# Performance work log

Hardware: AMD Instinct MI355X
Metric: run time of the kernel (lower is better)

Reference implementation:

```python
import jax, jax.numpy as jnp
import numpy as np

TOP_K = 2
EPS = 1e-6

def setup_inputs() -> dict:
    key = jax.random.key(0)
    ks = jax.random.split(key, 4)
    B, L, D, E, ED = 2, 2048, 2048, 8, 2048
    scale_gu = (6.0 / D) ** 0.5   # kaiming_uniform-ish bound
    scale_dn = (6.0 / ED) ** 0.5
    return {
        "x": jax.random.normal(ks[0], (B, L, D), jnp.float32),
        "router_scale": jnp.ones((D,), jnp.float32),
        "gate_w": jax.random.normal(ks[1], (D, E), jnp.float32) * (D ** -0.5),
        "gate_up": jax.random.uniform(ks[2], (E, D, 2 * ED), jnp.float32, -scale_gu, scale_gu),
        "down": jax.random.uniform(ks[3], (E, ED, D), jnp.float32, -scale_dn, scale_dn),
        "per_expert_scale": jnp.ones((E,), jnp.float32),
    }

def reference(x, router_scale, gate_w, gate_up, down, per_expert_scale):
    B, L, D = x.shape
    E = gate_up.shape[0]
    # --- Router: RMSNorm (no scale) * D^-0.5 * router_scale -> linear -> softmax -> topk -> renorm
    h = x * jax.lax.rsqrt(jnp.mean(x * x, axis=-1, keepdims=True) + EPS)
    h = h * (D ** -0.5) * router_scale
    logits = (h @ gate_w).astype(jnp.float32)            # [B,L,E]
    probs = jax.nn.softmax(logits, axis=-1)
    w, idx = jax.lax.top_k(probs, TOP_K)                 # [B,L,K]
    w = w / jnp.clip(jnp.sum(w, axis=-1, keepdims=True), 1e-12)
    w = w.astype(x.dtype)
    # --- Experts: dense compute over all experts, weighted combine by routing
    N = B * L
    xf = x.reshape(N, D)
    idxf = idx.reshape(N, TOP_K)
    wf = w.reshape(N, TOP_K)
    # combine[n,e] = sum_k wf[n,k] * (idxf[n,k]==e); top_k indices are distinct per token
    combine = jnp.zeros((N, E), x.dtype).at[jnp.arange(N)[:, None], idxf].add(wf)
    hh = jnp.einsum('nd,edf->nef', xf, gate_up)          # [N,E,2*ED]
    gate, up = jnp.split(hh, 2, axis=-1)
    act = jax.nn.gelu(gate, approximate=False) * up      # [N,E,ED]
    y = jnp.einsum('nef,efd->ned', act, down)            # [N,E,D]
    out = jnp.einsum('ne,ned->nd', combine * per_expert_scale, y)
    return out.reshape(B, L, D)
```

## Files before the change

### kernel.cpp

```cpp
#include <hip/hip_runtime.h>
#include <hip/hip_bf16.h>
#include <math.h>

#define NTOK 4096
#define DM   2048
#define NE   8
#define BK2  32
#define NT   64
#define TILE_BYTES 32768
#define B_OFF      16384

using f32x4  = float __attribute__((ext_vector_type(4)));
using bf16x8 = __bf16 __attribute__((ext_vector_type(8)));
using u32x4  = unsigned int __attribute__((ext_vector_type(4)));

#define SBAR()  __builtin_amdgcn_s_barrier()
#define SCHED() __builtin_amdgcn_sched_barrier(0)

__device__ __forceinline__ unsigned short bf16bits(float f){
  unsigned u = __builtin_bit_cast(unsigned, f);
  return (unsigned short)((u + 0x7fffu + ((u >> 16) & 1u)) >> 16);
}

__device__ __forceinline__ void load_lds16(const void* g, void* l){
  __builtin_amdgcn_global_load_lds(
      (const __attribute__((address_space(1))) unsigned int*)g,
      (__attribute__((address_space(3))) unsigned int*)l, 16, 0, 0);
}

__global__ __launch_bounds__(256) void router_kernel(
    const float* __restrict__ x, const float* __restrict__ rs,
    const float* __restrict__ gw, const float* __restrict__ pes,
    unsigned short* __restrict__ xbf, int* __restrict__ cnt,
    int* __restrict__ toklist, float* __restrict__ slotw,
    int* __restrict__ tok2slot)
{
  const int wv = threadIdx.x >> 6, l = threadIdx.x & 63;
  const int n = blockIdx.x * 4 + wv;
  const float* xr = x + (size_t)n * DM;
  unsigned short* xb = xbf + (size_t)n * DM;
  float ssq = 0.f;
  float lg[8] = {0,0,0,0,0,0,0,0};
  #pragma unroll
  for (int q = 0; q < 8; ++q){
    int c4 = l + 64 * q;
    float4 v = ((const float4*)xr)[c4];
    float4 r = ((const float4*)rs)[c4];
    ssq += v.x*v.x + v.y*v.y + v.z*v.z + v.w*v.w;
    ushort4 o; o.x = bf16bits(v.x); o.y = bf16bits(v.y); o.z = bf16bits(v.z); o.w = bf16bits(v.w);
    ((ushort4*)xb)[c4] = o;
    float xs0 = v.x*r.x, xs1 = v.y*r.y, xs2 = v.z*r.z, xs3 = v.w*r.w;
    const float4* gp = (const float4*)(gw + (size_t)c4 * 32);
    float4 ga, gb;
    ga = gp[0]; gb = gp[1];
    lg[0]+=xs0*ga.x; lg[1]+=xs0*ga.y; lg[2]+=xs0*ga.z; lg[3]+=xs0*ga.w;
    lg[4]+=xs0*gb.x; lg[5]+=xs0*gb.y; lg[6]+=xs0*gb.z; lg[7]+=xs0*gb.w;
    ga = gp[2]; gb = gp[3];
    lg[0]+=xs1*ga.x; lg[1]+=xs1*ga.y; lg[2]+=xs1*ga.z; lg[3]+=xs1*ga.w;
    lg[4]+=xs1*gb.x; lg[5]+=xs1*gb.y; lg[6]+=xs1*gb.z; lg[7]+=xs1*gb.w;
    ga = gp[4]; gb = gp[5];
    lg[0]+=xs2*ga.x; lg[1]+=xs2*ga.y; lg[2]+=xs2*ga.z; lg[3]+=xs2*ga.w;
    lg[4]+=xs2*gb.x; lg[5]+=xs2*gb.y; lg[6]+=xs2*gb.z; lg[7]+=xs2*gb.w;
    ga = gp[6]; gb = gp[7];
    lg[0]+=xs3*ga.x; lg[1]+=xs3*ga.y; lg[2]+=xs3*ga.z; lg[3]+=xs3*ga.w;
    lg[4]+=xs3*gb.x; lg[5]+=xs3*gb.y; lg[6]+=xs3*gb.z; lg[7]+=xs3*gb.w;
  }
  #pragma unroll
  for (int off = 32; off; off >>= 1){
    ssq += __shfl_xor(ssq, off, 64);
    #pragma unroll
    for (int e2 = 0; e2 < 8; ++e2) lg[e2] += __shfl_xor(lg[e2], off, 64);
  }
  if (l == 0){
    float c = rsqrtf(ssq * (1.0f/DM) + 1e-6f) * 0.022097086912079608f;
    float mx = -1e30f;
    #pragma unroll
    for (int e2 = 0; e2 < 8; ++e2){ lg[e2] *= c; mx = fmaxf(mx, lg[e2]); }
    float l0 = lg[0]; int i0 = 0;
    #pragma unroll
    for (int e2 = 1; e2 < 8; ++e2) if (lg[e2] > l0){ l0 = lg[e2]; i0 = e2; }
    int i1 = (i0 == 0) ? 1 : 0; float l1 = (i0 == 0) ? lg[1] : lg[0];
    #pragma unroll
    for (int e2 = 0; e2 < 8; ++e2){ if (e2 != i0 && lg[e2] > l1){ l1 = lg[e2]; i1 = e2; } }
    float p0 = expf(l0 - mx), p1 = expf(l1 - mx);
    float sw = fmaxf(p0 + p1, 1e-12f);
    float w0 = p0 / sw, w1 = p1 / sw;
    int s0 = atomicAdd(&cnt[i0], 1);
    toklist[i0 * NTOK + s0] = n;
    slotw[i0 * NTOK + s0] = w0 * pes[i0];
    tok2slot[2 * n] = (i0 << 16) | s0;
    int s1 = atomicAdd(&cnt[i1], 1);
    toklist[i1 * NTOK + s1] = n;
    slotw[i1 * NTOK + s1] = w1 * pes[i1];
    tok2slot[2 * n + 1] = (i1 << 16) | s1;
  }
}

__global__ void scan_kernel(const int* __restrict__ cnt, int* __restrict__ basep){
  if (threadIdx.x == 0){
    int a = 0;
    for (int e = 0; e < NE; ++e){ basep[e] = a; a += cnt[e]; }
  }
}

__global__ __launch_bounds__(256) void conv_transpose_kernel(
    const float* __restrict__ W, unsigned short* __restrict__ Wt, int ncols)
{
  const int z = blockIdx.z;
  const float* src = W + (size_t)z * 2048 * ncols;
  unsigned short* dst = Wt + (size_t)z * ncols * 2048;
  const int n0 = blockIdx.x * 64, k0 = blockIdx.y * 64;
  __shared__ __align__(16) unsigned short t[64][72];
  const int tid = threadIdx.x;
  const int kl = tid >> 4;
  const int nl = (tid & 15) * 4;
  #pragma unroll
  for (int q = 0; q < 4; ++q){
    int k = kl + q * 16;
    float4 v = *(const float4*)(src + (size_t)(k0 + k) * ncols + n0 + nl);
    t[nl+0][k] = bf16bits(v.x);
    t[nl+1][k] = bf16bits(v.y);
    t[nl+2][k] = bf16bits(v.z);
    t[nl+3][k] = bf16bits(v.w);
  }
  __syncthreads();
  const int nr = tid >> 3;
  const int k8 = (tid & 7) * 8;
  #pragma unroll
  for (int q = 0; q < 2; ++q){
    int n = nr + q * 32;
    u32x4 v = *(const u32x4*)&t[n][k8];
    *(u32x4*)(dst + (size_t)(n0 + n) * 2048 + k0 + k8) = v;
  }
}

template<int MODE>
__global__ __launch_bounds__(512, 1) void moe_gemm(
    const unsigned short* __restrict__ Abuf,
    const unsigned short* __restrict__ Wt,
    unsigned short* __restrict__ act,
    unsigned short* __restrict__ ybuf,
    const int* __restrict__ cnt,
    const int* __restrict__ basep,
    const int* __restrict__ toklist,
    int e0)
{
  const int gx = gridDim.x, gy = gridDim.y, gz = gridDim.z;
  int flat = blockIdx.x + gx * (blockIdx.y + gy * blockIdx.z);
  int per  = (gx * gy * gz) >> 3;
  int id2  = (flat & 7) * per + (flat >> 3);
  int fpb  = gy * gz;
  int fbi  = id2 / fpb;
  int rem  = id2 % fpb;
  const int z  = rem / gy;
  const int e  = e0 + z;
  const int ce = cnt[e];
  const int m0 = (rem % gy) * 256;
  if (m0 >= ce) return;
  const int fb = fbi * (MODE == 0 ? 128 : 256);
  const int tid = threadIdx.x;
  const int l = tid & 63;
  const int wv = tid >> 6;
  const int wr = wv >> 2;
  const int wc = wv & 3;
  const int baseE = basep[e];
  const size_t ncols = (MODE == 0) ? 4096 : 2048;
  const unsigned short* Wz = Wt + (size_t)z * ncols * 2048;

  __shared__ __align__(16) unsigned short smem[4 * TILE_BYTES / 2];

  const unsigned short* asrc[2];
  #pragma unroll
  for (int q = 0; q < 2; ++q){
    int r = q * 128 + (tid >> 2);
    int g = (tid & 3) ^ ((r >> 1) & 3);
    long rsrc;
    if (MODE == 0) rsrc = toklist[e * NTOK + min(m0 + r, ce - 1)];
    else           rsrc = baseE + min(m0 + r, ce - 1);
    asrc[q] = Abuf + (size_t)rsrc * 2048 + g * 8;
  }
  const unsigned short* bsrc[2];
  #pragma unroll
  for (int q = 0; q < 2; ++q){
    int col = q * 128 + (tid >> 2);
    int g = (tid & 3) ^ ((col >> 1) & 3);
    int n;
    if (MODE == 0){ int sub = col & 63; n = fb + (col >> 6) * 32 + (sub & 31) + ((sub & 32) ? 2048 : 0); }
    else n = fb + col;
    bsrc[q] = Wz + (size_t)n * 2048 + g * 8;
  }
  const int ldst = tid * 16;

  const int kq = l >> 4;
  const int swz = (kq ^ (((l & 15) >> 1) & 3)) * 16;
  const int abase = (wr * 128 + (l & 15)) * 64 + swz;
  const int bbase = B_OFF + (wc * 64 + (l & 15)) * 64 + swz;

  f32x4 acc[8][4];
  #pragma unroll
  for (int i = 0; i < 8; ++i)
    #pragma unroll
    for (int j = 0; j < 4; ++j)
      acc[i][j] = (f32x4){0.f, 0.f, 0.f, 0.f};

  auto stage_a = [&](int buf, int st){
    char* base = (char*)smem + buf * TILE_BYTES;
    load_lds16(asrc[0] + st * BK2, base + ldst);
    load_lds16(asrc[1] + st * BK2, base + 8192 + ldst);
  };
  auto stage_b = [&](int buf, int st){
    char* base = (char*)smem + buf * TILE_BYTES + B_OFF;
    load_lds16(bsrc[0] + st * BK2, base + ldst);
    load_lds16(bsrc[1] + st * BK2, base + 8192 + ldst);
  };

  stage_a(0, 0); stage_b(0, 0);
  stage_a(1, 1); stage_b(1, 1);
  stage_a(2, 2); stage_b(2, 2);
  asm volatile("s_waitcnt vmcnt(8)");
  SCHED();
  SBAR();
  SCHED();

  #pragma unroll 1
  for (int kt = 0; kt < NT; ++kt){
    const char* C = (const char*)smem + (kt & 3) * TILE_BYTES;
    const int sb = (kt + 3) & 3;
    const int st = min(kt + 3, NT - 1);
    bf16x8 af[4], bfr[4];
    #pragma unroll
    for (int ni = 0; ni < 4; ++ni) bfr[ni] = *(const bf16x8*)(C + bbase + ni * 1024);
    #pragma unroll
    for (int mi = 0; mi < 4; ++mi) af[mi] = *(const bf16x8*)(C + abase + mi * 1024);
    stage_a(sb, st);
    SCHED();
    SBAR();
    SCHED();
    __builtin_amdgcn_s_setprio(1);
    #pragma unroll
    for (int ni = 0; ni < 4; ++ni)
      #pragma unroll
      for (int mi = 0; mi < 4; ++mi)
        acc[mi][ni] = __builtin_amdgcn_mfma_f32_16x16x32_bf16(af[mi], bfr[ni], acc[mi][ni], 0, 0, 0);
    __builtin_amdgcn_s_setprio(0);
    SCHED();
    SBAR();
    SCHED();
    #pragma unroll
    for (int mi = 0; mi < 4; ++mi) af[mi] = *(const bf16x8*)(C + abase + (mi + 4) * 1024);
    stage_b(sb, st);
    SCHED();
    SBAR();
    SCHED();
    __builtin_amdgcn_s_setprio(1);
    #pragma unroll
    for (int ni = 0; ni < 4; ++ni)
      #pragma unroll
      for (int mi = 0; mi < 4; ++mi)
        acc[mi + 4][ni] = __builtin_amdgcn_mfma_f32_16x16x32_bf16(af[mi], bfr[ni], acc[mi + 4][ni], 0, 0, 0);
    __builtin_amdgcn_s_setprio(0);
    SCHED();
    asm volatile("s_waitcnt vmcnt(8)");
    SCHED();
    SBAR();
    SCHED();
  }
  asm volatile("s_waitcnt vmcnt(0)");
  SCHED();

  const int lq4 = (l >> 4) * 4;
  if (MODE == 0){
    #pragma unroll
    for (int mi = 0; mi < 8; ++mi)
      #pragma unroll
      for (int j = 0; j < 4; ++j){
        int s = m0 + wr * 128 + mi * 16 + lq4 + j;
        if (s < ce){
          size_t rowb = (size_t)(baseE + s) * 2048;
          #pragma unroll
          for (int p = 0; p < 2; ++p){
            float g = acc[mi][p][j];
            float u = acc[mi][p + 2][j];
            float a = 0.5f * g * (1.0f + erff(g * 0.70710678118654752f)) * u;
            act[rowb + fb + wc * 32 + p * 16 + (l & 15)] = bf16bits(a);
          }
        }
      }
  } else {
    #pragma unroll
    for (int mi = 0; mi < 8; ++mi)
      #pragma unroll
      for (int j = 0; j < 4; ++j){
        int s = m0 + wr * 128 + mi * 16 + lq4 + j;
        if (s < ce){
          unsigned short* yr = ybuf + (size_t)(baseE + s) * 2048 + fb + wc * 64 + (l & 15);
          #pragma unroll
          for (int ni = 0; ni < 4; ++ni)
            yr[ni * 16] = bf16bits(acc[mi][ni][j]);
        }
      }
  }
}

__global__ __launch_bounds__(256) void combine_kernel(
    const unsigned short* __restrict__ ybuf, const int* __restrict__ tok2slot,
    const float* __restrict__ slotw, const int* __restrict__ basep,
    float* __restrict__ out)
{
  const int n = blockIdx.x * 4 + (threadIdx.x >> 6);
  const int l = threadIdx.x & 63;
  int p0 = tok2slot[2 * n], p1 = tok2slot[2 * n + 1];
  int e0 = p0 >> 16, s0 = p0 & 0xffff;
  int e1 = p1 >> 16, s1 = p1 & 0xffff;
  float w0 = slotw[e0 * NTOK + s0], w1 = slotw[e1 * NTOK + s1];
  const unsigned short* y0 = ybuf + (size_t)(basep[e0] + s0) * 2048;
  const unsigned short* y1 = ybuf + (size_t)(basep[e1] + s1) * 2048;
  float* o = out + (size_t)n * 2048;
  #pragma unroll
  for (int q = 0; q < 4; ++q){
    int c8 = (l + 64 * q) * 8;
    u32x4 a = *(const u32x4*)(y0 + c8);
    u32x4 b = *(const u32x4*)(y1 + c8);
    float rr[8];
    #pragma unroll
    for (int i = 0; i < 4; ++i){
      float a0 = __builtin_bit_cast(float, a[i] << 16);
      float a1 = __builtin_bit_cast(float, a[i] & 0xffff0000u);
      float b0 = __builtin_bit_cast(float, b[i] << 16);
      float b1 = __builtin_bit_cast(float, b[i] & 0xffff0000u);
      rr[2*i]   = w0 * a0 + w1 * b0;
      rr[2*i+1] = w0 * a1 + w1 * b1;
    }
    float4 v0 = {rr[0], rr[1], rr[2], rr[3]};
    float4 v1 = {rr[4], rr[5], rr[6], rr[7]};
    *(float4*)(o + c8) = v0;
    *(float4*)(o + c8 + 4) = v1;
  }
}

extern "C" void kernel_launch(void* const* d_in, const int* in_sizes, int n_in,
                              void* d_out, int out_size, void* d_ws, size_t ws_size,
                              hipStream_t stream)
{
  const float* x   = (const float*)d_in[0];
  const float* rs  = (const float*)d_in[1];
  const float* gw  = (const float*)d_in[2];
  const float* w1  = (const float*)d_in[3];
  const float* w2  = (const float*)d_in[4];
  const float* pes = (const float*)d_in[5];
  float* out = (float*)d_out;

  char* ws = (char*)d_ws;
  int*   cnt      = (int*)ws;
  int*   basep    = (int*)(ws + 64);
  int*   toklist  = (int*)(ws + 256);
  float* slotw    = (float*)(ws + 256 + (size_t)NE * NTOK * 4);
  int*   tok2slot = (int*)(ws + 256 + 2 * (size_t)NE * NTOK * 4);
  unsigned short* xbf  = (unsigned short*)(ws + 256 + 2 * (size_t)NE * NTOK * 4 + (size_t)NTOK * 8);
  unsigned short* act  = xbf + (size_t)NTOK * DM;
  unsigned short* ybuf = act + (size_t)2 * NTOK * DM;
  unsigned short* wtb  = ybuf + (size_t)2 * NTOK * DM;

  const size_t fixed = (size_t)((char*)wtb - ws);
  const size_t per_e = (size_t)4096 * 2048 * 2;
  int EG = NE;
  while (EG > 1 && fixed + (size_t)EG * per_e > ws_size) EG >>= 1;

  hipMemsetAsync(cnt, 0, 64, stream);
  router_kernel<<<NTOK / 4, 256, 0, stream>>>(x, rs, gw, pes, xbf, cnt, toklist, slotw, tok2slot);
  scan_kernel<<<1, 64, 0, stream>>>(cnt, basep);

  for (int g = 0; g < NE; g += EG){
    conv_transpose_kernel<<<dim3(64, 32, EG), 256, 0, stream>>>(
        w1 + (size_t)g * 2048 * 4096, wtb, 4096);
    moe_gemm<0><<<dim3(16, 16, EG), 512, 0, stream>>>(
        xbf, wtb, act, ybuf, cnt, basep, toklist, g);
  }
  for (int g = 0; g < NE; g += EG){
    conv_transpose_kernel<<<dim3(32, 32, EG), 256, 0, stream>>>(
        w2 + (size_t)g * 2048 * 2048, wtb, 2048);
    moe_gemm<1><<<dim3(8, 16, EG), 512, 0, stream>>>(
        act, wtb, act, ybuf, cnt, basep, toklist, g);
  }
  combine_kernel<<<NTOK / 4, 256, 0, stream>>>(ybuf, tok2slot, slotw, basep, out);
}
```

Measured before the change: 574.8 us.

## Restructure MoE GEMM into double-buffered 64-wide K tiles with asm LDS reads

The GEMM main loop changes from a four-slot ring of 32-wide K tiles to two buffers, each holding a 64-wide K tile split into two A pieces and two B pieces. Each iteration now runs four MFMA phases with explicit lgkmcnt waits. LDS reads become inline-asm ds_read_b128 with precomputed swizzled offsets and immediate displacements, which cuts address arithmetic. The XCD-aware block-index remapping is dropped in favour of direct blockIdx mapping, which may hurt L2 locality. Launch bounds now ask for two blocks per CU, which caps registers around the 128-register accumulator and risks spills, while 128KB of LDS per block likely still allows only one block.

```diff
diff --git a/kernel.cpp b/kernel.cpp
--- a/kernel.cpp
+++ b/kernel.cpp
@@ -5,10 +5,7 @@
 #define NTOK 4096
 #define DM   2048
 #define NE   8
-#define BK2  32
-#define NT   64
-#define TILE_BYTES 32768
-#define B_OFF      16384
+#define NKT  32
 
 using f32x4  = float __attribute__((ext_vector_type(4)));
 using bf16x8 = __bf16 __attribute__((ext_vector_type(8)));
@@ -26,6 +23,18 @@
   __builtin_amdgcn_global_load_lds(
       (const __attribute__((address_space(1))) unsigned int*)g,
       (__attribute__((address_space(3))) unsigned int*)l, 16, 0, 0);
+}
+
+__device__ __forceinline__ unsigned lds_addr(const void* p){
+  return (unsigned)(unsigned long long)
+      (__attribute__((address_space(3))) const char*)p;
+}
+
+template<int IMM>
+__device__ __forceinline__ bf16x8 lds_read16(unsigned addr){
+  u32x4 r;
+  asm volatile("ds_read_b128 %0, %1 offset:%c2" : "=v"(r) : "v"(addr), "i"(IMM));
+  return __builtin_bit_cast(bf16x8, r);
 }
 
 __global__ __launch_bounds__(256) void router_kernel(
@@ -135,7 +144,7 @@
 }
 
 template<int MODE>
-__global__ __launch_bounds__(512, 1) void moe_gemm(
+__global__ __launch_bounds__(512, 2) void moe_gemm(
     const unsigned short* __restrict__ Abuf,
     const unsigned short* __restrict__ Wt,
     unsigned short* __restrict__ act,
@@ -145,19 +154,11 @@
     const int* __restrict__ toklist,
     int e0)
 {
-  const int gx = gridDim.x, gy = gridDim.y, gz = gridDim.z;
-  int flat = blockIdx.x + gx * (blockIdx.y + gy * blockIdx.z);
-  int per  = (gx * gy * gz) >> 3;
-  int id2  = (flat & 7) * per + (flat >> 3);
-  int fpb  = gy * gz;
-  int fbi  = id2 / fpb;
-  int rem  = id2 % fpb;
-  const int z  = rem / gy;
-  const int e  = e0 + z;
+  const int z = blockIdx.z, e = e0 + z;
   const int ce = cnt[e];
-  const int m0 = (rem % gy) * 256;
+  const int m0 = blockIdx.y * 256;
   if (m0 >= ce) return;
-  const int fb = fbi * (MODE == 0 ? 128 : 256);
+  const int fb = blockIdx.x * (MODE == 0 ? 128 : 256);
   const int tid = threadIdx.x;
   const int l = tid & 63;
   const int wv = tid >> 6;
@@ -167,34 +168,52 @@
   const size_t ncols = (MODE == 0) ? 4096 : 2048;
   const unsigned short* Wz = Wt + (size_t)z * ncols * 2048;
 
-  __shared__ __align__(16) unsigned short smem[4 * TILE_BYTES / 2];
-
-  const unsigned short* asrc[2];
+  __shared__ __align__(16) unsigned char smem[2][4][16384];
+
+  const unsigned short* asrcp[2];
+  const unsigned short* bsrcp[2];
   #pragma unroll
   for (int q = 0; q < 2; ++q){
-    int r = q * 128 + (tid >> 2);
-    int g = (tid & 3) ^ ((r >> 1) & 3);
+    int c = q * 512 + tid;
+    int rl = c >> 2;
+    int gl = (c & 3) ^ ((rl >> 1) & 3);
     long rsrc;
-    if (MODE == 0) rsrc = toklist[e * NTOK + min(m0 + r, ce - 1)];
-    else           rsrc = baseE + min(m0 + r, ce - 1);
-    asrc[q] = Abuf + (size_t)rsrc * 2048 + g * 8;
-  }
-  const unsigned short* bsrc[2];
-  #pragma unroll
-  for (int q = 0; q < 2; ++q){
-    int col = q * 128 + (tid >> 2);
-    int g = (tid & 3) ^ ((col >> 1) & 3);
+    if (MODE == 0) rsrc = toklist[e * NTOK + min(m0 + rl, ce - 1)];
+    else           rsrc = baseE + min(m0 + rl, ce - 1);
+    asrcp[q] = Abuf + (size_t)rsrc * 2048 + gl * 8;
     int n;
-    if (MODE == 0){ int sub = col & 63; n = fb + (col >> 6) * 32 + (sub & 31) + ((sub & 32) ? 2048 : 0); }
-    else n = fb + col;
-    bsrc[q] = Wz + (size_t)n * 2048 + g * 8;
-  }
-  const int ldst = tid * 16;
-
+    if (MODE == 0) n = fb + (rl >> 6) * 32 + (rl & 31) + ((rl & 32) ? 2048 : 0);
+    else           n = fb + rl;
+    bsrcp[q] = Wz + (size_t)n * 2048 + gl * 8;
+  }
+  const int dst16 = tid * 16;
+
+  auto stage = [&](int buf, int piece, int isB, int ksrc){
+    unsigned char* base = &smem[buf][piece][0];
+    if (isB){
+      load_lds16(bsrcp[0] + ksrc, base + dst16);
+      load_lds16(bsrcp[1] + ksrc, base + 8192 + dst16);
+    } else {
+      load_lds16(asrcp[0] + ksrc, base + dst16);
+      load_lds16(asrcp[1] + ksrc, base + 8192 + dst16);
+    }
+  };
+
+  const unsigned lbase = lds_addr(&smem[0][0][0]);
   const int kq = l >> 4;
-  const int swz = (kq ^ (((l & 15) >> 1) & 3)) * 16;
-  const int abase = (wr * 128 + (l & 15)) * 64 + swz;
-  const int bbase = B_OFF + (wc * 64 + (l & 15)) * 64 + swz;
+  unsigned aoffs[2][4], boffs[4];
+  #pragma unroll
+  for (int h = 0; h < 2; ++h)
+    #pragma unroll
+    for (int m = 0; m < 4; ++m){
+      int row = wr * 128 + h * 64 + m * 16 + (l & 15);
+      aoffs[h][m] = row * 64 + (unsigned)((kq ^ ((row >> 1) & 3)) * 16);
+    }
+  #pragma unroll
+  for (int n = 0; n < 4; ++n){
+    int col = wc * 64 + n * 16 + (l & 15);
+    boffs[n] = col * 64 + (unsigned)((kq ^ ((col >> 1) & 3)) * 16);
+  }
 
   f32x4 acc[8][4];
   #pragma unroll
@@ -203,70 +222,106 @@
     for (int j = 0; j < 4; ++j)
       acc[i][j] = (f32x4){0.f, 0.f, 0.f, 0.f};
 
-  auto stage_a = [&](int buf, int st){
-    char* base = (char*)smem + buf * TILE_BYTES;
-    load_lds16(asrc[0] + st * BK2, base + ldst);
-    load_lds16(asrc[1] + st * BK2, base + 8192 + ldst);
-  };
-  auto stage_b = [&](int buf, int st){
-    char* base = (char*)smem + buf * TILE_BYTES + B_OFF;
-    load_lds16(bsrc[0] + st * BK2, base + ldst);
-    load_lds16(bsrc[1] + st * BK2, base + 8192 + ldst);
-  };
-
-  stage_a(0, 0); stage_b(0, 0);
-  stage_a(1, 1); stage_b(1, 1);
-  stage_a(2, 2); stage_b(2, 2);
+  stage(0, 0, 0, 0);
+  stage(0, 2, 1, 0);
+  stage(0, 1, 0, 32);
+  stage(0, 3, 1, 32);
+  stage(1, 0, 0, 64);
+  stage(1, 2, 1, 64);
+  SCHED();
   asm volatile("s_waitcnt vmcnt(8)");
   SCHED();
   SBAR();
   SCHED();
 
   #pragma unroll 1
-  for (int kt = 0; kt < NT; ++kt){
-    const char* C = (const char*)smem + (kt & 3) * TILE_BYTES;
-    const int sb = (kt + 3) & 3;
-    const int st = min(kt + 3, NT - 1);
-    bf16x8 af[4], bfr[4];
-    #pragma unroll
-    for (int ni = 0; ni < 4; ++ni) bfr[ni] = *(const bf16x8*)(C + bbase + ni * 1024);
-    #pragma unroll
-    for (int mi = 0; mi < 4; ++mi) af[mi] = *(const bf16x8*)(C + abase + mi * 1024);
-    stage_a(sb, st);
-    SCHED();
-    SBAR();
-    SCHED();
-    __builtin_amdgcn_s_setprio(1);
-    #pragma unroll
-    for (int ni = 0; ni < 4; ++ni)
-      #pragma unroll
-      for (int mi = 0; mi < 4; ++mi)
-        acc[mi][ni] = __builtin_amdgcn_mfma_f32_16x16x32_bf16(af[mi], bfr[ni], acc[mi][ni], 0, 0, 0);
-    __builtin_amdgcn_s_setprio(0);
-    SCHED();
-    SBAR();
-    SCHED();
-    #pragma unroll
-    for (int mi = 0; mi < 4; ++mi) af[mi] = *(const bf16x8*)(C + abase + (mi + 4) * 1024);
-    stage_b(sb, st);
-    SCHED();
-    SBAR();
-    SCHED();
-    __builtin_amdgcn_s_setprio(1);
-    #pragma unroll
-    for (int ni = 0; ni < 4; ++ni)
-      #pragma unroll
-      for (int mi = 0; mi < 4; ++mi)
-        acc[mi + 4][ni] = __builtin_amdgcn_mfma_f32_16x16x32_bf16(af[mi], bfr[ni], acc[mi + 4][ni], 0, 0, 0);
-    __builtin_amdgcn_s_setprio(0);
-    SCHED();
-    asm volatile("s_waitcnt vmcnt(8)");
-    SCHED();
-    SBAR();
-    SCHED();
+  for (int kt = 0; kt < NKT; ++kt){
+    const int buf = kt & 1;
+    const unsigned cb = lbase + (unsigned)buf * 65536;
+    int kA1 = (kt + 1) * 64 + 32; if (kA1 > 2016) kA1 = 2016;
+    int kN0 = (kt + 2) * 64;      if (kN0 > 2016) kN0 = 2016;
+    bf16x8 bfr[4];
+
+    {
+      bf16x8 af[4];
+      #pragma unroll
+      for (int m = 0; m < 4; ++m) af[m] = lds_read16<0>(cb + aoffs[0][m]);
+      #pragma unroll
+      for (int n = 0; n < 4; ++n) bfr[n] = lds_read16<32768>(cb + boffs[n]);
+      stage(buf ^ 1, 1, 0, kA1);
+      SCHED(); SBAR();
+      asm volatile("s_waitcnt lgkmcnt(0)");
+      SCHED();
+      __builtin_amdgcn_s_setprio(1);
+      #pragma unroll
+      for (int n = 0; n < 4; ++n)
+        #pragma unroll
+        for (int m = 0; m < 4; ++m)
+          acc[m][n] = __builtin_amdgcn_mfma_f32_16x16x32_bf16(af[m], bfr[n], acc[m][n], 0, 0, 0);
+      __builtin_amdgcn_s_setprio(0);
+      SCHED(); SBAR(); SCHED();
+    }
+    {
+      bf16x8 af[4];
+      #pragma unroll
+      for (int m = 0; m < 4; ++m) af[m] = lds_read16<0>(cb + aoffs[1][m]);
+      stage(buf ^ 1, 3, 1, kA1);
+      SCHED(); SBAR();
+      asm volatile("s_waitcnt lgkmcnt(0)");
+      SCHED();
+      __builtin_amdgcn_s_setprio(1);
+      #pragma unroll
+      for (int n = 0; n < 4; ++n)
+        #pragma unroll
+        for (int m = 0; m < 4; ++m)
+          acc[4 + m][n] = __builtin_amdgcn_mfma_f32_16x16x32_bf16(af[m], bfr[n], acc[4 + m][n], 0, 0, 0);
+      __builtin_amdgcn_s_setprio(0);
+      SCHED();
+      asm volatile("s_waitcnt vmcnt(8)");
+      SCHED(); SBAR(); SCHED();
+    }
+    {
+      bf16x8 af[4];
+      #pragma unroll
+      for (int m = 0; m < 4; ++m) af[m] = lds_read16<16384>(cb + aoffs[0][m]);
+      #pragma unroll
+      for (int n = 0; n < 4; ++n) bfr[n] = lds_read16<49152>(cb + boffs[n]);
+      stage(buf, 0, 0, kN0);
+      SCHED(); SBAR();
+      asm volatile("s_waitcnt lgkmcnt(0)");
+      SCHED();
+      __builtin_amdgcn_s_setprio(1);
+      #pragma unroll
+      for (int n = 0; n < 4; ++n)
+        #pragma unroll
+        for (int m = 0; m < 4; ++m)
+          acc[m][n] = __builtin_amdgcn_mfma_f32_16x16x32_bf16(af[m], bfr[n], acc[m][n], 0, 0, 0);
+      __builtin_amdgcn_s_setprio(0);
+      SCHED(); SBAR(); SCHED();
+    }
+    {
+      bf16x8 af[4];
+      #pragma unroll
+      for (int m = 0; m < 4; ++m) af[m] = lds_read16<16384>(cb + aoffs[1][m]);
+      stage(buf, 2, 1, kN0);
+      SCHED(); SBAR();
+      asm volatile("s_waitcnt lgkmcnt(0)");
+      SCHED();
+      __builtin_amdgcn_s_setprio(1);
+      #pragma unroll
+      for (int n = 0; n < 4; ++n)
+        #pragma unroll
+        for (int m = 0; m < 4; ++m)
+          acc[4 + m][n] = __builtin_amdgcn_mfma_f32_16x16x32_bf16(af[m], bfr[n], acc[4 + m][n], 0, 0, 0);
+      __builtin_amdgcn_s_setprio(0);
+      SCHED();
+      asm volatile("s_waitcnt vmcnt(8)");
+      SCHED(); SBAR(); SCHED();
+    }
   }
   asm volatile("s_waitcnt vmcnt(0)");
   SCHED();
+  SBAR();
 
   const int lq4 = (l >> 4) * 4;
   if (MODE == 0){
```

Result: faster. 528.7 us (-8.0%).
